# Kernel optimization log

Hardware: AMD Instinct MI355X
Metric: run time of the kernel (lower is better)

The kernel has to match this reference:

```python
import jax, jax.numpy as jnp
import numpy as np

B, S, H, E, K = 4, 2048, 1024, 8, 2


def setup_inputs() -> dict:
    key = jax.random.key(0)
    k0, k1, k2 = jax.random.split(key, 3)
    x = jax.random.normal(k0, (B, S, H), dtype=jnp.float32)
    # gate: Linear(H -> E); torch stores W as [out,in], we keep [E,H]
    gate_w = jax.random.normal(k1, (E, H), dtype=jnp.float32) * 0.02
    gate_b = jnp.zeros((E,), dtype=jnp.float32)
    # experts: E x Linear(H -> H); stored as [E, H_in, H_out]
    expert_w = jax.random.normal(k2, (E, H, H), dtype=jnp.float32) * 0.02
    expert_b = jnp.zeros((E, H), dtype=jnp.float32)
    return {"x": x, "gate_w": gate_w, "gate_b": gate_b,
            "expert_w": expert_w, "expert_b": expert_b}


def reference(x, gate_w, gate_b, expert_w, expert_b):
    bsz, seq_len, h = x.shape
    xt = x.reshape(-1, h)                      # [T, H]
    T = xt.shape[0]

    # router (moe_router): softmax -> top-k -> renormalize
    logits = xt @ gate_w.T + gate_b            # [T, E]
    routing_probs = jax.nn.softmax(logits, axis=-1)
    top_k_probs, top_k_index = jax.lax.top_k(routing_probs, K)
    top_k_probs = top_k_probs / jnp.sum(top_k_probs, axis=1, keepdims=True)
    top_k_probs = top_k_probs.astype(x.dtype)

    # combine weights: scatter normalized top-k probs into [T, E]
    rows = jnp.arange(T)[:, None]
    combine = jnp.zeros((T, E), dtype=x.dtype).at[rows, top_k_index].add(top_k_probs)

    # per-expert FFN over all tokens, then weighted combine
    # (equivalent math to the gather / index_add loop: zero weights contribute zero)
    y = jnp.einsum('th,eho->teo', xt, expert_w) + expert_b[None, :, :]  # [T, E, H]
    out = jnp.einsum('te,teh->th', combine, y)                          # [T, H]

    final_output = out.reshape(bsz, seq_len, h)
    return final_output, top_k_index, routing_probs
```

## Files before the change

### kernel.cpp

```cpp
#include <hip/hip_runtime.h>
#include <hip/hip_bf16.h>
#include <stdint.h>

typedef unsigned short ushort_t;
typedef __bf16 bf16x8 __attribute__((ext_vector_type(8)));
typedef float f32x4 __attribute__((ext_vector_type(4)));

#define T_TOK 8192
#define H_DIM 1024
#define E_EXP 8
#define BM 128
#define BN 128
#define BK 64
#define NKT (H_DIM / BK)
#define NWG_G 2304

#define CNT_STRIDE 64
#define RTOK 32
#define RBLOCKS (T_TOK / RTOK)
#define TP_BLOCKS ((H_DIM / 32) * (H_DIM / 32) * E_EXP)

static __device__ __forceinline__ ushort_t f2bf(float f) {
  union { float f; uint32_t u; } c; c.f = f;
  uint32_t u = c.u;
  uint32_t r = u + 0x7FFFu + ((u >> 16) & 1u);
  return (ushort_t)(r >> 16);
}

__global__ __launch_bounds__(256) void router_transpose(
    const float* __restrict__ x, const float* __restrict__ gw,
    const float* __restrict__ gb, const float* __restrict__ ew,
    float* __restrict__ out_idx, float* __restrict__ out_probs,
    int* __restrict__ counts, int* __restrict__ tok, float* __restrict__ wts,
    ushort_t* __restrict__ x_bf, ushort_t* __restrict__ wT)
{
  __shared__ int   sm_eid[RTOK * 2];
  __shared__ float sm_wt[RTOK * 2];
  __shared__ int   lcnt[E_EXP], lbase[E_EXP], lpos[E_EXP];
  __shared__ float tile[32][33];

  const int tid = threadIdx.x;

  if (blockIdx.x >= RBLOCKS) {
    const int tb = blockIdx.x - RBLOCKS;
    const int e = tb >> 10;
    const int n0 = (tb & 31) * 32, k0 = ((tb >> 5) & 31) * 32;
    const float* we = ew + (size_t)e * H_DIM * H_DIM;
    ushort_t* wTe = wT + (size_t)e * H_DIM * H_DIM;
    const int tx = tid & 31, ty = tid >> 5;
#pragma unroll
    for (int i = 0; i < 4; i++)
      tile[ty + 8 * i][tx] = we[(size_t)(k0 + ty + 8 * i) * H_DIM + n0 + tx];
    __syncthreads();
#pragma unroll
    for (int i = 0; i < 4; i++)
      wTe[(size_t)(n0 + ty + 8 * i) * H_DIM + k0 + tx] = f2bf(tile[tx][ty + 8 * i]);
    return;
  }

  const int wave = tid >> 6, l = tid & 63;
  if (tid < E_EXP) { lcnt[tid] = 0; lpos[tid] = 0; }
  __syncthreads();

  const int t0 = blockIdx.x * RTOK;
  for (int it = 0; it < RTOK / 4; it++) {
    const int lt = wave * (RTOK / 4) + it;
    const int t = t0 + lt;
    const float* xt = x + (size_t)t * H_DIM;
    float acc[E_EXP];
#pragma unroll
    for (int e = 0; e < E_EXP; e++) acc[e] = 0.f;
#pragma unroll
    for (int i = 0; i < 4; i++) {
      const int h = (i * 64 + l) * 4;
      const float4 xv = *reinterpret_cast<const float4*>(xt + h);
      ushort4 b;
      b.x = f2bf(xv.x); b.y = f2bf(xv.y); b.z = f2bf(xv.z); b.w = f2bf(xv.w);
      *reinterpret_cast<ushort4*>(x_bf + (size_t)t * H_DIM + h) = b;
#pragma unroll
      for (int e = 0; e < E_EXP; e++) {
        const float4 g = *reinterpret_cast<const float4*>(gw + e * H_DIM + h);
        acc[e] += xv.x * g.x + xv.y * g.y + xv.z * g.z + xv.w * g.w;
      }
    }
#pragma unroll
    for (int e = 0; e < E_EXP; e++) {
      float v = acc[e];
#pragma unroll
      for (int off = 32; off; off >>= 1) v += __shfl_xor(v, off);
      acc[e] = v;
    }
    if (l == 0) {
      float lg[E_EXP], pb[E_EXP];
      float m = -1e30f;
#pragma unroll
      for (int e = 0; e < E_EXP; e++) { lg[e] = acc[e] + gb[e]; m = fmaxf(m, lg[e]); }
      float s = 0.f;
#pragma unroll
      for (int e = 0; e < E_EXP; e++) { pb[e] = expf(lg[e] - m); s += pb[e]; }
      const float inv = 1.f / s;
#pragma unroll
      for (int e = 0; e < E_EXP; e++) {
        pb[e] *= inv;
        out_probs[(size_t)t * E_EXP + e] = pb[e];
      }
      int i0 = 0; float p0 = pb[0];
#pragma unroll
      for (int e = 1; e < E_EXP; e++) if (pb[e] > p0) { p0 = pb[e]; i0 = e; }
      int i1 = -1; float p1 = -1.f;
#pragma unroll
      for (int e = 0; e < E_EXP; e++) if (e != i0 && pb[e] > p1) { p1 = pb[e]; i1 = e; }
      out_idx[(size_t)t * 2 + 0] = (float)i0;
      out_idx[(size_t)t * 2 + 1] = (float)i1;
      const float rn = 1.f / (p0 + p1);
      sm_eid[lt * 2 + 0] = i0; sm_wt[lt * 2 + 0] = p0 * rn;
      sm_eid[lt * 2 + 1] = i1; sm_wt[lt * 2 + 1] = p1 * rn;
    }
  }
  __syncthreads();

  if (tid < RTOK * 2) atomicAdd(&lcnt[sm_eid[tid]], 1);
  __syncthreads();
  if (tid < E_EXP) lbase[tid] = atomicAdd(&counts[tid * CNT_STRIDE], lcnt[tid]);
  __syncthreads();
  if (tid < RTOK * 2) {
    const int e = sm_eid[tid];
    const int p = lbase[e] + atomicAdd(&lpos[e], 1);
    const int dst = e * T_TOK + p;
    tok[dst] = (t0 + (tid >> 1)) * 2 + (tid & 1);
    wts[dst] = sm_wt[tid];
  }
}

#define GLDS16(gp, lp)                                                         \
  __builtin_amdgcn_global_load_lds(                                            \
      (const __attribute__((address_space(1))) void*)(gp),                     \
      (__attribute__((address_space(3))) void*)(lp), 16, 0, 0)

__global__ __launch_bounds__(256, 3) void moe_gemm(
    const ushort_t* __restrict__ x_bf, const ushort_t* __restrict__ wT,
    const float* __restrict__ bias, int* __restrict__ counts,
    const int* __restrict__ tok, const float* __restrict__ wts,
    ushort_t* __restrict__ y)
{
  __shared__ __align__(16) ushort_t As[2 * 4096];
  __shared__ __align__(16) ushort_t Bs[2 * 4096];
  __shared__ int stok[BM];
  __shared__ float swt[BM];
  __shared__ int s_spill;

  const int tid = threadIdx.x;
  const int bid = blockIdx.x;

  int ne[E_EXP], fl[E_EXP];
#pragma unroll
  for (int i = 0; i < E_EXP; i++) {
    ne[i] = counts[i * CNT_STRIDE];
    fl[i] = ne[i] >> 7;
  }

  const int l = tid & 63;
  const int wid = tid >> 6;
  const int fr = l & 15;
  const int g = l >> 4;

  if (bid < 2048) {
    int e = bid & 7;
    int q = bid >> 3;
    const int home = fl[e] * 8;
    if (q >= (home < 256 ? home : 256)) {
      int sc[E_EXP], spill_total = 0;
#pragma unroll
      for (int i = 0; i < E_EXP; i++) {
        sc[i] = fl[i] * 8 > 256 ? fl[i] * 8 - 256 : 0;
        spill_total += sc[i];
      }
      if (spill_total == 0) return;
      if (tid == 0) s_spill = atomicAdd(&counts[520], 1);
      __syncthreads();
      int k = s_spill;
      if (k >= spill_total) return;
      int done = 0;
#pragma unroll
      for (int i = 0; i < E_EXP; i++) {
        if (!done) { if (k < sc[i]) { e = i; done = 1; } else k -= sc[i]; }
      }
      q = 256 + k;
    }
    const int mt = q >> 3;
    const int nt = q & 7;

    if (tid < BM) {
      stok[tid] = tok[e * T_TOK + mt * BM + tid];
      swt[tid] = wts[e * T_TOK + mt * BM + tid];
    }
    __syncthreads();

    const int r0 = tid >> 2;
    const int cp = (tid & 3) ^ ((tid >> 3) & 3);
    const ushort_t* wTe = wT + (size_t)e * H_DIM * H_DIM;
    const ushort_t* aP0 = x_bf + (size_t)(stok[r0] >> 1) * H_DIM + cp * 8;
    const ushort_t* aP1 = x_bf + (size_t)(stok[r0 + 64] >> 1) * H_DIM + cp * 8;
    const ushort_t* bP0 = wTe + (size_t)(nt * BN + r0) * H_DIM + cp * 8;
    const ushort_t* bP1 = wTe + (size_t)(nt * BN + r0 + 64) * H_DIM + cp * 8;
    const int d0 = tid * 8;
    const int d1 = (tid + 256) * 8;

#define STAGE8(t)                                                              \
  do {                                                                         \
    GLDS16(aP0 + (t) * BK +  0, &As[0 * 4096 + d0]);                           \
    GLDS16(aP1 + (t) * BK +  0, &As[0 * 4096 + d1]);                           \
    GLDS16(aP0 + (t) * BK + 32, &As[1 * 4096 + d0]);                           \
    GLDS16(aP1 + (t) * BK + 32, &As[1 * 4096 + d1]);                           \
    GLDS16(bP0 + (t) * BK +  0, &Bs[0 * 4096 + d0]);                           \
    GLDS16(bP1 + (t) * BK +  0, &Bs[0 * 4096 + d1]);                           \
    GLDS16(bP0 + (t) * BK + 32, &Bs[1 * 4096 + d0]);                           \
    GLDS16(bP1 + (t) * BK + 32, &Bs[1 * 4096 + d1]);                           \
  } while (0)

    const int wm = wid >> 1, wn = wid & 1;
    const int sl = g ^ ((l >> 1) & 3);
    const int arow0 = wm * 64 + fr;
    const int brow0 = wn * 64 + fr;

    f32x4 acc[4][4] = {};

#pragma unroll 1
    for (int t = 0; t < NKT; ++t) {
      if (t) __syncthreads();
      STAGE8(t);
      __syncthreads();
#pragma unroll
      for (int kk = 0; kk < 2; kk++) {
        bf16x8 af[4], bv[4];
#pragma unroll
        for (int mi = 0; mi < 4; mi++)
          af[mi] = *reinterpret_cast<const bf16x8*>(
              &As[kk * 4096 + (arow0 + mi * 16) * 32 + sl * 8]);
#pragma unroll
        for (int nj = 0; nj < 4; nj++)
          bv[nj] = *reinterpret_cast<const bf16x8*>(
              &Bs[kk * 4096 + (brow0 + nj * 16) * 32 + sl * 8]);
        __builtin_amdgcn_s_setprio(1);
#pragma unroll
        for (int mi = 0; mi < 4; mi++)
#pragma unroll
          for (int nj = 0; nj < 4; nj++)
            acc[mi][nj] = __builtin_amdgcn_mfma_f32_16x16x32_bf16(
                af[mi], bv[nj], acc[mi][nj], 0, 0, 0);
        __builtin_amdgcn_s_setprio(0);
      }
    }

    float bias4[4];
#pragma unroll
    for (int nj = 0; nj < 4; nj++)
      bias4[nj] = bias[e * H_DIM + nt * BN + wn * 64 + nj * 16 + fr];
#pragma unroll
    for (int mi = 0; mi < 4; mi++) {
      const int rr0 = wm * 64 + mi * 16 + g * 4;
#pragma unroll
      for (int r = 0; r < 4; r++) {
        const int row = rr0 + r;
        const float wgt = swt[row];
        ushort_t* yr = y + (size_t)stok[row] * H_DIM;
#pragma unroll
        for (int nj = 0; nj < 4; nj++) {
          const int n = nt * BN + wn * 64 + nj * 16 + fr;
          yr[n] = f2bf(wgt * (acc[mi][nj][r] + bias4[nj]));
        }
      }
    }
  } else {
    const int e = bid & 7;
    const int tq = (bid - 2048) >> 3;
    const int rem = ne[e] - (fl[e] << 7);
    const int tcnt = (rem + 63) >> 6;
    if (tq >= tcnt * 8) return;
    const int mtt = tq >> 3;
    const int ntt = tq & 7;
    const int row0 = (fl[e] << 7) + mtt * 64;
    int valid = ne[e] - row0; if (valid > 64) valid = 64;

    if (tid < 64) {
      int slot = row0 + tid;
      if (slot >= ne[e]) slot = ne[e] - 1;
      stok[tid] = tok[e * T_TOK + slot];
      swt[tid] = wts[e * T_TOK + slot];
    }
    __syncthreads();

    const ushort_t* wTe = wT + (size_t)e * H_DIM * H_DIM;
    const int trow = tid >> 3;
    const int tlc = (tid & 7) ^ (trow & 7);
    const ushort_t* taS0 = x_bf + (size_t)(stok[trow] >> 1) * H_DIM + tlc * 8;
    const ushort_t* taS1 = x_bf + (size_t)(stok[trow + 32] >> 1) * H_DIM + tlc * 8;
    const ushort_t* tbS0 = wTe + (size_t)(ntt * 128 + trow) * H_DIM + tlc * 8;
    const ushort_t* tbS1 = tbS0 + (size_t)32 * H_DIM;
    const ushort_t* tbS2 = tbS0 + (size_t)64 * H_DIM;
    const ushort_t* tbS3 = tbS0 + (size_t)96 * H_DIM;

#define TSTAGE1(t)                                                             \
  do {                                                                         \
    GLDS16(taS0 + (t) * BK, &As[tid * 8]);                                     \
    GLDS16(taS1 + (t) * BK, &As[(tid + 256) * 8]);                             \
    GLDS16(tbS0 + (t) * BK, &Bs[tid * 8]);                                     \
    GLDS16(tbS1 + (t) * BK, &Bs[(tid + 256) * 8]);                             \
    GLDS16(tbS2 + (t) * BK, &Bs[(tid + 512) * 8]);                             \
    GLDS16(tbS3 + (t) * BK, &Bs[(tid + 768) * 8]);                             \
  } while (0)

    const int tph0 = (g ^ (fr & 7)) * 8;
    const int tph1 = ((4 ^ g) ^ (fr & 7)) * 8;

    f32x4 tacc[2][4] = {};

#pragma unroll 1
    for (int t = 0; t < NKT; ++t) {
      if (t) __syncthreads();
      TSTAGE1(t);
      __syncthreads();
#pragma unroll
      for (int kk = 0; kk < 2; kk++) {
        const int ph = kk ? tph1 : tph0;
#pragma unroll
        for (int nf = 0; nf < 2; nf++) {
          const bf16x8 tbv = *reinterpret_cast<const bf16x8*>(
              &Bs[(wid * 32 + nf * 16 + fr) * 64 + ph]);
#pragma unroll
          for (int mi = 0; mi < 4; mi++) {
            const bf16x8 tav = *reinterpret_cast<const bf16x8*>(
                &As[(mi * 16 + fr) * 64 + ph]);
            tacc[nf][mi] = __builtin_amdgcn_mfma_f32_16x16x32_bf16(
                tav, tbv, tacc[nf][mi], 0, 0, 0);
          }
        }
      }
    }

#pragma unroll
    for (int nf = 0; nf < 2; nf++) {
      const int ncol = ntt * 128 + wid * 32 + nf * 16 + fr;
      const float bs = bias[e * H_DIM + ncol];
#pragma unroll
      for (int mi = 0; mi < 4; mi++) {
        const int rb = mi * 16 + g * 4;
#pragma unroll
        for (int r = 0; r < 4; r++) {
          const int row = rb + r;
          if (row < valid) {
            ushort_t* yr = y + (size_t)stok[row] * H_DIM;
            yr[ncol] = f2bf(swt[row] * (tacc[nf][mi][r] + bs));
          }
        }
      }
    }
  }
}

__global__ __launch_bounds__(256) void combine_kernel(
    const ushort_t* __restrict__ y, float* __restrict__ out)
{
  const int t = blockIdx.x;
  const ushort_t* r0 = y + (size_t)(t * 2) * H_DIM;
  const ushort_t* r1 = r0 + H_DIM;
  float* o = out + (size_t)t * H_DIM;
  const int h = threadIdx.x * 4;
  const ushort4 u0 = *reinterpret_cast<const ushort4*>(r0 + h);
  const ushort4 u1 = *reinterpret_cast<const ushort4*>(r1 + h);
  float4 v;
  union { uint32_t u; float f; } c;
  c.u = (uint32_t)u0.x << 16; v.x = c.f; c.u = (uint32_t)u1.x << 16; v.x += c.f;
  c.u = (uint32_t)u0.y << 16; v.y = c.f; c.u = (uint32_t)u1.y << 16; v.y += c.f;
  c.u = (uint32_t)u0.z << 16; v.z = c.f; c.u = (uint32_t)u1.z << 16; v.z += c.f;
  c.u = (uint32_t)u0.w << 16; v.w = c.f; c.u = (uint32_t)u1.w << 16; v.w += c.f;
  *reinterpret_cast<float4*>(o + h) = v;
}

extern "C" void kernel_launch(void* const* d_in, const int* in_sizes, int n_in,
                              void* d_out, int out_size, void* d_ws, size_t ws_size,
                              hipStream_t stream)
{
  const float* x  = (const float*)d_in[0];
  const float* gw = (const float*)d_in[1];
  const float* gb = (const float*)d_in[2];
  const float* ew = (const float*)d_in[3];
  const float* eb = (const float*)d_in[4];

  float* out = (float*)d_out;
  float* out_final = out;
  float* out_idx   = out + (size_t)T_TOK * H_DIM;
  float* out_probs = out_idx + (size_t)T_TOK * 2;

  char* ws = (char*)d_ws;
  size_t off = 0;
  int*      counts  = (int*)(ws + off); off += 4096;
  int*      tok     = (int*)(ws + off); off += (size_t)E_EXP * T_TOK * 4;
  float*    wts     = (float*)(ws + off); off += (size_t)E_EXP * T_TOK * 4;
  ushort_t* x_bf    = (ushort_t*)(ws + off); off += (size_t)T_TOK * H_DIM * 2;
  ushort_t* wT      = (ushort_t*)(ws + off); off += (size_t)E_EXP * H_DIM * H_DIM * 2;
  ushort_t* y       = (ushort_t*)(ws + off); off += (size_t)T_TOK * 2 * H_DIM * 2;

  hipMemsetAsync(counts, 0, 4096, stream);

  router_transpose<<<RBLOCKS + TP_BLOCKS, 256, 0, stream>>>(
      x, gw, gb, ew, out_idx, out_probs, counts, tok, wts, x_bf, wT);
  moe_gemm<<<NWG_G, 256, 0, stream>>>(x_bf, wT, eb, counts, tok, wts, y);
  combine_kernel<<<T_TOK, 256, 0, stream>>>(y, out_final);
}
```

Before: 93.72 us.

## Stage GEMM epilogue through LDS for coalesced 16-byte stores; reorder tail blocks first

The expert GEMM epilogue now writes the bf16 results into shared memory, then copies each 128-column row slice to the scattered token rows of y with 16-byte vector stores. The old code issued scattered 2-byte stores. The tail-tile blocks are also moved to the low block indices so they are scheduled before the main tiles. The cost is two extra barriers and an LDS round trip per tile.

After: 91.72 us. 2.1% less time.

```diff
diff --git a/kernel.cpp b/kernel.cpp
--- a/kernel.cpp
+++ b/kernel.cpp
@@ -164,9 +164,9 @@
   const int fr = l & 15;
   const int g = l >> 4;
 
-  if (bid < 2048) {
+  if (bid >= 256) {
     int e = bid & 7;
-    int q = bid >> 3;
+    int q = (bid - 256) >> 3;
     const int home = fl[e] * 8;
     if (q >= (home < 256 ? home : 256)) {
       int sc[E_EXP], spill_total = 0;
@@ -252,6 +252,7 @@
       }
     }
 
+    __syncthreads();
     float bias4[4];
 #pragma unroll
     for (int nj = 0; nj < 4; nj++)
@@ -263,17 +264,29 @@
       for (int r = 0; r < 4; r++) {
         const int row = rr0 + r;
         const float wgt = swt[row];
-        ushort_t* yr = y + (size_t)stok[row] * H_DIM;
 #pragma unroll
         for (int nj = 0; nj < 4; nj++) {
-          const int n = nt * BN + wn * 64 + nj * 16 + fr;
-          yr[n] = f2bf(wgt * (acc[mi][nj][r] + bias4[nj]));
+          const int col = wn * 64 + nj * 16 + fr;
+          const ushort_t v = f2bf(wgt * (acc[mi][nj][r] + bias4[nj]));
+          if (row < 64) As[row * 128 + col] = v;
+          else          Bs[(row - 64) * 128 + col] = v;
         }
       }
+    }
+    __syncthreads();
+#pragma unroll
+    for (int i = 0; i < 8; i++) {
+      const int c = tid + i * 256;
+      const int row = c >> 4;
+      const int ci = c & 15;
+      const ushort_t* src = (row < 64) ? &As[row * 128 + ci * 8]
+                                       : &Bs[(row - 64) * 128 + ci * 8];
+      ushort_t* dst = y + (size_t)stok[row] * H_DIM + nt * BN + ci * 8;
+      *reinterpret_cast<int4*>(dst) = *reinterpret_cast<const int4*>(src);
     }
   } else {
     const int e = bid & 7;
-    const int tq = (bid - 2048) >> 3;
+    const int tq = bid >> 3;
     const int rem = ne[e] - (fl[e] << 7);
     const int tcnt = (rem + 63) >> 6;
     if (tq >= tcnt * 8) return;
@@ -338,21 +351,34 @@
       }
     }
 
+    __syncthreads();
+    float bs2[2];
+#pragma unroll
+    for (int nf = 0; nf < 2; nf++)
+      bs2[nf] = bias[e * H_DIM + ntt * 128 + wid * 32 + nf * 16 + fr];
 #pragma unroll
     for (int nf = 0; nf < 2; nf++) {
-      const int ncol = ntt * 128 + wid * 32 + nf * 16 + fr;
-      const float bs = bias[e * H_DIM + ncol];
+      const int col = wid * 32 + nf * 16 + fr;
 #pragma unroll
       for (int mi = 0; mi < 4; mi++) {
         const int rb = mi * 16 + g * 4;
 #pragma unroll
         for (int r = 0; r < 4; r++) {
           const int row = rb + r;
-          if (row < valid) {
-            ushort_t* yr = y + (size_t)stok[row] * H_DIM;
-            yr[ncol] = f2bf(swt[row] * (tacc[nf][mi][r] + bs));
-          }
+          As[row * 128 + col] = f2bf(swt[row] * (tacc[nf][mi][r] + bs2[nf]));
         }
+      }
+    }
+    __syncthreads();
+#pragma unroll
+    for (int i = 0; i < 4; i++) {
+      const int c = tid + i * 256;
+      const int row = c >> 4;
+      const int ci = c & 15;
+      if (row < valid) {
+        ushort_t* dst = y + (size_t)stok[row] * H_DIM + ntt * 128 + ci * 8;
+        *reinterpret_cast<int4*>(dst) =
+            *reinterpret_cast<const int4*>(&As[row * 128 + ci * 8]);
       }
     }
   }
```
